# Kernel optimization log

Hardware: AMD Instinct MI355X
Metric: run time of the kernel (lower is better)

## Reference

```python
import jax, jax.numpy as jnp
import numpy as np

B, T, I, H, NC = 128, 512, 128, 512, 100


def setup_inputs() -> dict:
    key = jax.random.key(0)
    ks = jax.random.split(key, 16)
    x = jax.random.randint(ks[0], (B, T, 1), 0, NC + 1)
    # embedding table with padding row 0 zeroed (padding_idx=0)
    emb = (jax.random.normal(ks[1], (NC + 1, I)) * 1.0).at[0].set(0.0)
    # kaiming_normal_ fan_out, sigmoid nonlinearity -> std = 1/sqrt(fan_out)
    sx = 1.0 / np.sqrt(H)
    sc = 1.0 / np.sqrt(H)
    sp = 1.0 / np.sqrt(NC)
    return {
        "x": x,
        "emb": emb,
        "Wfx": jax.random.normal(ks[2], (I, H)) * sx,
        "Wfc": jax.random.normal(ks[3], (H, H)) * sc,
        "bf": jnp.zeros((H,)),
        "Wix": jax.random.normal(ks[4], (I, H)) * sx,
        "Wic": jax.random.normal(ks[5], (H, H)) * sc,
        "bi": jnp.zeros((H,)),
        "Wox": jax.random.normal(ks[6], (I, H)) * sx,
        "Woc": jax.random.normal(ks[7], (H, H)) * sc,
        "bo": jnp.zeros((H,)),
        "Wcx": jax.random.normal(ks[8], (I, H)) * sx,
        "bc": jnp.zeros((H,)),
        "Wph": jax.random.normal(ks[9], (H, NC)) * sp,
        "bp": jnp.zeros((NC,)),
    }


def reference(x, emb, Wfx, Wfc, bf, Wix, Wic, bi, Wox, Woc, bo, Wcx, bc, Wph, bp):
    idx = x[:, :, 0]                      # [B,T] int indices
    xe = emb[idx]                         # [B,T,I] embedded inputs
    h_dim = Wfc.shape[0]
    # Fuse the four input-side GEMMs into one, hoisted out of the recurrence.
    Wx = jnp.concatenate([Wfx, Wix, Wox, Wcx], axis=1)   # [I,4H]
    bx = jnp.concatenate([bf, bi, bo, bc])               # [4H]
    xg = jnp.einsum('bti,ih->bth', xe, Wx) + bx          # [B,T,4H]
    # Fuse the three peephole (cell-state) GEMMs into one per step.
    Wc = jnp.concatenate([Wfc, Wic, Woc], axis=1)        # [H,3H]
    reset = (idx > 0).astype(xg.dtype)                   # [B,T]

    def step(carry, inp):
        C, h = carry
        g, r = inp                        # g: [B,4H], r: [B]
        cg = C @ Wc                       # [B,3H]
        f = jax.nn.sigmoid(g[:, :h_dim] + cg[:, :h_dim])
        i = jax.nn.sigmoid(g[:, h_dim:2 * h_dim] + cg[:, h_dim:2 * h_dim])
        o = jax.nn.sigmoid(g[:, 2 * h_dim:3 * h_dim] + cg[:, 2 * h_dim:])
        c_tilde = jax.nn.sigmoid(g[:, 3 * h_dim:])        # note: sigmoid, not tanh (per source)
        Cn = (c_tilde * i + C * f) * r[:, None]           # reset on padding tokens
        hn = jnp.tanh(Cn) * o
        return (Cn, hn), None

    bsz = xg.shape[0]
    init = (jnp.zeros((bsz, h_dim), xg.dtype), jnp.zeros((bsz, h_dim), xg.dtype))
    xs = (jnp.swapaxes(xg, 0, 1), jnp.swapaxes(reset, 0, 1))  # time-major
    (Cf, hf), _ = jax.lax.scan(step, init, xs)
    p = hf @ Wph + bp                     # [B,num_classes]
    return jax.nn.log_softmax(p, axis=1)
```

## Files before the change

kernel.cpp:

```cpp
#include <hip/hip_runtime.h>
#include <hip/hip_bf16.h>
#include <stdint.h>

#define HD   512
#define ID   128
#define NCLS 100
#define TT   512
#define BB   128
#define NEMB 101
#define THR  512

#define NGRPF 32
#define GWGF  8
#define RPGF  4
#define COLSF 64
#define NGRPB 64
#define GWGB  4
#define RPGB  2
#define COLSB 128

#define CPAD 640
#define CBW  260
#define PROW 2056
#define PSTB 3

#define WS_FLAG 0
#define WS_BAR  4096
#define WS_G    65536
#define WS_C0   (1u * 1024 * 1024)
#define WS_C1   (WS_C0 + 262144)
#define WS_HFB  (WS_C1 + 262144)
#define NBARU   4096
#define NCU     65536

using bf16 = __hip_bfloat16;

__device__ __forceinline__ float b2f(bf16 v) { return __bfloat162float(v); }
__device__ __forceinline__ float sigf(float x) { return 1.0f / (1.0f + expf(-x)); }

__device__ __forceinline__ float cld(const float* p) {
    return __hip_atomic_load(p, __ATOMIC_RELAXED, __HIP_MEMORY_SCOPE_AGENT);
}
__device__ __forceinline__ void cst(float* p, float v) {
    __hip_atomic_store(p, v, __ATOMIC_RELAXED, __HIP_MEMORY_SCOPE_AGENT);
}
__device__ __forceinline__ void cstu(uint32_t* p, uint32_t v) {
    __hip_atomic_store(p, v, __ATOMIC_RELAXED, __HIP_MEMORY_SCOPE_AGENT);
}
__device__ __forceinline__ uint32_t cldu(const uint32_t* p) {
    return __hip_atomic_load(p, __ATOMIC_RELAXED, __HIP_MEMORY_SCOPE_AGENT);
}
__device__ __forceinline__ uint64_t cldu8(const uint64_t* p) {
    return __hip_atomic_load(p, __ATOMIC_RELAXED, __HIP_MEMORY_SCOPE_AGENT);
}

__device__ __forceinline__ uint32_t pkbf(float x, float y) {
    uint32_t u;
    asm("v_cvt_pk_bf16_f32 %0, %1, %2" : "=v"(u) : "v"(x), "v"(y));
    return u;
}
#define DOT2(acc, w, c) \
    asm("v_dot2_f32_bf16 %0, %1, %2, %0" : "+v"(acc) : "v"(w), "v"(c))

template <bool BF>
__device__ __forceinline__ float ldv(const void* p, int i) {
    if constexpr (BF) return b2f(((const bf16*)p)[i]);
    else              return ((const float*)p)[i];
}

__device__ __forceinline__ int cpi(int h) { return (h >> 4) * 20 + (h & 15); }

__device__ __forceinline__ void gbarrier(unsigned* cnt, unsigned* iter, int gwg) {
    __syncthreads();
    if (threadIdx.x == 0) {
        __hip_atomic_fetch_add(cnt, 1u, __ATOMIC_RELAXED, __HIP_MEMORY_SCOPE_AGENT);
        const unsigned tgt = (*iter + 1u) * (unsigned)gwg;
        while (__hip_atomic_load(cnt, __ATOMIC_RELAXED, __HIP_MEMORY_SCOPE_AGENT) < tgt)
            ;
    }
    ++*iter;
    __syncthreads();
}

__global__ void init_k(const uint32_t* __restrict__ emb_raw,
                       int* __restrict__ flag, unsigned* __restrict__ bars,
                       uint32_t* __restrict__ c0, uint32_t* __restrict__ c1) {
    const int t = blockIdx.x * 1024 + threadIdx.x;
    for (int k = t; k < NBARU; k += 8192) bars[k] = 0u;
    for (int k = t; k < NCU; k += 8192) { c0[k] = 0u; c1[k] = 0u; }
    if (t == 0) {
        uint32_t acc = 0;
        for (int i = 64; i < 128; ++i) acc |= emb_raw[i];
        *flag = (acc == 0u) ? 0 : 1;
    }
}

template <bool BF>
__device__ __forceinline__ void build_G_body(
    const void* emb, const void* Wfx, const void* Wix,
    const void* Wox, const void* Wcx,
    const void* bfv, const void* biv, const void* bov, const void* bcv,
    float* G) {
    const int c   = blockIdx.x;
    const int j   = blockIdx.y * 256 + threadIdx.x;
    const int q   = j >> 9;
    const int col = j & 511;
    const void* W  = (q == 0) ? Wfx : (q == 1) ? Wix : (q == 2) ? Wox : Wcx;
    const void* bv = (q == 0) ? bfv : (q == 1) ? biv : (q == 2) ? bov : bcv;
    float acc = ldv<BF>(bv, col);
    #pragma unroll 4
    for (int i = 0; i < ID; ++i)
        acc += ldv<BF>(emb, c * ID + i) * ldv<BF>(W, i * HD + col);
    if (q == 3) acc = sigf(acc);
    G[c * 2048 + j] = acc;
}

__global__ void build_G_k(const int* __restrict__ flag,
                          const void* __restrict__ emb,
                          const void* __restrict__ Wfx, const void* __restrict__ Wix,
                          const void* __restrict__ Wox, const void* __restrict__ Wcx,
                          const void* __restrict__ bfv, const void* __restrict__ biv,
                          const void* __restrict__ bov, const void* __restrict__ bcv,
                          float* __restrict__ G) {
    if (*flag == 0) build_G_body<false>(emb, Wfx, Wix, Wox, Wcx, bfv, biv, bov, bcv, G);
    else            build_G_body<true >(emb, Wfx, Wix, Wox, Wcx, bfv, biv, bov, bcv, G);
}

__global__ __launch_bounds__(THR, 2) void recur_bs(
    const int* __restrict__ flag, const int* __restrict__ x,
    const float* __restrict__ G,
    const void* __restrict__ Wfc, const void* __restrict__ Wic,
    const void* __restrict__ Woc,
    float* __restrict__ C0, float* __restrict__ C1,
    float* __restrict__ Hfb, unsigned* __restrict__ bars)
{
    __shared__ __align__(16) float Cs[RPGF * CPAD];
    __shared__ __align__(16) uint32_t CbS[RPGB * CBW];
    __shared__ __align__(8)  float2 part2[2 * RPGF * PROW];
    __shared__ int idx[RPGF * TT];
    __shared__ int lz[RPGF];

    const int blk = blockIdx.x;
    const int tid = threadIdx.x;
    unsigned bi = 0;
    const int fl = *flag;

    if (fl == 0) {
        const int grp   = blk >> 3;
        const int rank  = blk & 7;
        const int r0    = grp * RPGF;
        const int h0    = rank * COLSF;
        const int cp    = tid & 15;
        const int chunk = tid >> 4;
        unsigned* bar = bars + grp * 32;

        idx[tid]        = x[r0 * TT + tid];
        idx[tid + 512]  = x[r0 * TT + tid + 512];
        idx[tid + 1024] = x[r0 * TT + tid + 1024];
        idx[tid + 1536] = x[r0 * TT + tid + 1536];
        for (int k = tid; k < RPGF * CPAD; k += THR) Cs[k] = 0.0f;
        if (tid < RPGF) lz[tid] = -1;
        __syncthreads();
        #pragma unroll
        for (int r = 0; r < RPGF; ++r)
            if (idx[r * TT + tid] == 0) atomicMax(&lz[r], tid);
        __syncthreads();
        int t0 = TT;
        #pragma unroll
        for (int r = 0; r < RPGF; ++r) t0 = min(t0, lz[r] + 1);

        float wf0[16], wf1[16], wf2[16], wf3[16];
        float wi0[16], wi1[16], wi2[16], wi3[16];
        #pragma unroll
        for (int k = 0; k < 16; ++k) {
            const int hp = chunk * 16 + k;
            wf0[k] = ldv<false>(Wfc, hp * HD + h0 + cp);
            wf1[k] = ldv<false>(Wfc, hp * HD + h0 + cp + 16);
            wf2[k] = ldv<false>(Wfc, hp * HD + h0 + cp + 32);
            wf3[k] = ldv<false>(Wfc, hp * HD + h0 + cp + 48);
            wi0[k] = ldv<false>(Wic, hp * HD + h0 + cp);
            wi1[k] = ldv<false>(Wic, hp * HD + h0 + cp + 16);
            wi2[k] = ldv<false>(Wic, hp * HD + h0 + cp + 32);
            wi3[k] = ldv<false>(Wic, hp * HD + h0 + cp + 48);
        }
        #pragma unroll
        for (int k = 0; k < 16; ++k)
            asm volatile("" : "+v"(wf0[k]), "+v"(wf1[k]), "+v"(wf2[k]), "+v"(wf3[k]),
                              "+v"(wi0[k]), "+v"(wi1[k]), "+v"(wi2[k]), "+v"(wi3[k]));

        const bool isUpd = (tid < COLSF * RPGF);
        const int uc = tid & 63, ur = tid >> 6;
        const int pe = cpi(tid);

        {
            uint32_t* tA = (uint32_t*)((t0 & 1) ? C1 : C0);
            uint32_t* tB = (uint32_t*)((t0 & 1) ? C0 : C1);
            if (isUpd) {
                cstu(tA + (r0 + ur) * HD + h0 + uc, (uint32_t)(t0 & 3));
                cstu(tB + (r0 + ur) * HD + h0 + uc, (uint32_t)((t0 + 3) & 3));
            }
        }
        gbarrier(bar, &bi, GWGF);

        float Creg = 0.0f;
        for (int t = t0; t < TT; ++t) {
            #pragma unroll
            for (int k = 0; k < 16; ++k)
                asm volatile("" : "+v"(wf0[k]), "+v"(wf1[k]), "+v"(wf2[k]), "+v"(wf3[k]),
                                  "+v"(wi0[k]), "+v"(wi1[k]), "+v"(wi2[k]), "+v"(wi3[k]));

            const uint32_t* curT = (const uint32_t*)((t & 1) ? C1 : C0);
            uint32_t*       nxtT = (uint32_t*)((t & 1) ? C0 : C1);

            float gf = 0.f, gi = 0.f, sgc = 0.f;
            int cl = 1;
            if (isUpd) {
                cl = idx[ur * TT + t];
                const float* Gr = G + cl * 2048;
                gf  = Gr[h0 + uc];
                gi  = Gr[512 + h0 + uc];
                sgc = Gr[1536 + h0 + uc];
            }

            {
                const uint32_t* s0 = curT + (r0 + 0) * HD + tid;
                const uint32_t* s1 = curT + (r0 + 1) * HD + tid;
                const uint32_t* s2 = curT + (r0 + 2) * HD + tid;
                const uint32_t* s3 = curT + (r0 + 3) * HD + tid;
                const uint32_t exp = (uint32_t)t & 3u;
                uint32_t w0, w1, w2, w3;
                do { w0 = cldu(s0); } while ((w0 ^ exp) & 3u);
                for (;;) {
                    w1 = cldu(s1); w2 = cldu(s2); w3 = cldu(s3);
                    if ((((w1 ^ exp) | (w2 ^ exp) | (w3 ^ exp)) & 3u) == 0u)
                        break;
                }
                Cs[0 * CPAD + pe] = __uint_as_float(w0 & ~3u);
                Cs[1 * CPAD + pe] = __uint_as_float(w1 & ~3u);
                Cs[2 * CPAD + pe] = __uint_as_float(w2 & ~3u);
                Cs[3 * CPAD + pe] = __uint_as_float(w3 & ~3u);
            }
            asm volatile("s_waitcnt lgkmcnt(0)" ::: "memory");

            float f0[RPGF], f1[RPGF], f2[RPGF], f3[RPGF];
            float i0[RPGF], i1[RPGF], i2[RPGF], i3[RPGF];
            #pragma unroll
            for (int r = 0; r < RPGF; ++r) {
                f0[r] = 0.f; f1[r] = 0.f; f2[r] = 0.f; f3[r] = 0.f;
                i0[r] = 0.f; i1[r] = 0.f; i2[r] = 0.f; i3[r] = 0.f;
            }
            {
                const int cb = chunk * 5;
                #pragma unroll
                for (int j = 0; j < 4; ++j) {
                    #pragma unroll
                    for (int r = 0; r < RPGF; ++r) {
                        const float4 cv = reinterpret_cast<const float4*>(
                            Cs + r * CPAD)[cb + j];
                        f0[r] += wf0[4*j]*cv.x + wf0[4*j+1]*cv.y + wf0[4*j+2]*cv.z + wf0[4*j+3]*cv.w;
                        f1[r] += wf1[4*j]*cv.x + wf1[4*j+1]*cv.y + wf1[4*j+2]*cv.z + wf1[4*j+3]*cv.w;
                        f2[r] += wf2[4*j]*cv.x + wf2[4*j+1]*cv.y + wf2[4*j+2]*cv.z + wf2[4*j+3]*cv.w;
                        f3[r] += wf3[4*j]*cv.x + wf3[4*j+1]*cv.y + wf3[4*j+2]*cv.z + wf3[4*j+3]*cv.w;
                        i0[r] += wi0[4*j]*cv.x + wi0[4*j+1]*cv.y + wi0[4*j+2]*cv.z + wi0[4*j+3]*cv.w;
                        i1[r] += wi1[4*j]*cv.x + wi1[4*j+1]*cv.y + wi1[4*j+2]*cv.z + wi1[4*j+3]*cv.w;
                        i2[r] += wi2[4*j]*cv.x + wi2[4*j+1]*cv.y + wi2[4*j+2]*cv.z + wi2[4*j+3]*cv.w;
                        i3[r] += wi3[4*j]*cv.x + wi3[4*j+1]*cv.y + wi3[4*j+2]*cv.z + wi3[4*j+3]*cv.w;
                    }
                }
            }

            {
                float2* Pb = part2 + (t & 1) * (RPGF * PROW);
                #pragma unroll
                for (int r = 0; r < RPGF; ++r) {
                    float2* Pr = Pb + r * PROW + chunk * 64;
                    Pr[cp]      = make_float2(f0[r], i0[r]);
                    Pr[cp + 16] = make_float2(f1[r], i1[r]);
                    Pr[cp + 32] = make_float2(f2[r], i2[r]);
                    Pr[cp + 48] = make_float2(f3[r], i3[r]);
                }
            }
            __syncthreads();

            if (isUpd) {
                const float2* Pr = part2 + (t & 1) * (RPGF * PROW) + ur * PROW;
                float df = 0.f, di = 0.f;
                #pragma unroll
                for (int ch = 0; ch < 32; ++ch) {
                    const float2 v = Pr[ch * 64 + uc];
                    df += v.x;
                    di += v.y;
                }
                float Cn = sgc * sigf(gi + di) + Creg * sigf(gf + df);
                Cn = (cl > 0) ? Cn : 0.0f;
                Creg = Cn;
                cstu(nxtT + (r0 + ur) * HD + h0 + uc,
                     (__float_as_uint(Cn) & ~3u) | ((uint32_t)(t + 1) & 3u));
            }
        }

        __syncthreads();
        {
            const int oc = tid & 63, och = tid >> 6;
            float ao[RPGF];
            #pragma unroll
            for (int r = 0; r < RPGF; ++r) ao[r] = 0.0f;
            #pragma unroll 4
            for (int k = 0; k < 64; ++k) {
                const int hp = och * 64 + k;
                const int hpp = cpi(hp);
                const float wo = ldv<false>(Woc, hp * HD + h0 + oc);
                #pragma unroll
                for (int r = 0; r < RPGF; ++r)
                    ao[r] += wo * Cs[r * CPAD + hpp];
            }
            {
                #pragma unroll
                for (int r2 = 0; r2 < RPGF / 2; ++r2)
                    part2[r2 * PROW + och * 64 + oc] =
                        make_float2(ao[2 * r2], ao[2 * r2 + 1]);
            }
            __syncthreads();
            if (isUpd) {
                const float2* Pr = part2 + (ur >> 1) * PROW;
                float s = 0.f;
                #pragma unroll
                for (int ch = 0; ch < 8; ++ch) {
                    const float2 v = Pr[ch * 64 + uc];
                    s += (ur & 1) ? v.y : v.x;
                }
                const int cl2 = idx[ur * TT + TT - 1];
                const float o = sigf(G[cl2 * 2048 + 1024 + h0 + uc] + s);
                Hfb[(r0 + ur) * HD + h0 + uc] = tanhf(Creg) * o;
            }
        }
    } else {
        const int grp   = blk >> 2;
        const int rank  = blk & 3;
        const int r0    = grp * RPGB;
        const int h0    = rank * COLSB;
        const int cp    = tid & 31;
        const int chunk = tid >> 5;

        idx[tid]       = x[r0 * TT + tid];
        idx[tid + 512] = x[r0 * TT + tid + 512];
        for (int k = tid; k < RPGB * CBW; k += THR) CbS[k] = 0u;
        if (tid < RPGB) lz[tid] = -1;
        __syncthreads();
        #pragma unroll
        for (int r = 0; r < RPGB; ++r)
            if (idx[r * TT + tid] == 0) atomicMax(&lz[r], tid);
        __syncthreads();
        int t0 = TT;
        #pragma unroll
        for (int r = 0; r < RPGB; ++r) t0 = min(t0, lz[r] + 1);

        const uint16_t* Wfr = (const uint16_t*)Wfc;
        const uint16_t* Wir = (const uint16_t*)Wic;
        uint32_t wf0[16], wf1[16], wf2[16], wf3[16];
        uint32_t wi0[16], wi1[16], wi2[16], wi3[16];
        #pragma unroll
        for (int p = 0; p < 16; ++p) {
            const int hp = chunk * 32 + 2 * p;
            const int b0 = hp * HD + h0 + cp, b1 = (hp + 1) * HD + h0 + cp;
            wf0[p] = (uint32_t)Wfr[b0]      | ((uint32_t)Wfr[b1]      << 16);
            wf1[p] = (uint32_t)Wfr[b0 + 32] | ((uint32_t)Wfr[b1 + 32] << 16);
            wf2[p] = (uint32_t)Wfr[b0 + 64] | ((uint32_t)Wfr[b1 + 64] << 16);
            wf3[p] = (uint32_t)Wfr[b0 + 96] | ((uint32_t)Wfr[b1 + 96] << 16);
            wi0[p] = (uint32_t)Wir[b0]      | ((uint32_t)Wir[b1]      << 16);
            wi1[p] = (uint32_t)Wir[b0 + 32] | ((uint32_t)Wir[b1 + 32] << 16);
            wi2[p] = (uint32_t)Wir[b0 + 64] | ((uint32_t)Wir[b1 + 64] << 16);
            wi3[p] = (uint32_t)Wir[b0 + 96] | ((uint32_t)Wir[b1 + 96] << 16);
        }
        #pragma unroll
        for (int p = 0; p < 16; ++p)
            asm volatile("" : "+v"(wf0[p]), "+v"(wf1[p]), "+v"(wf2[p]), "+v"(wf3[p]),
                              "+v"(wi0[p]), "+v"(wi1[p]), "+v"(wi2[p]), "+v"(wi3[p]));

        const bool isUpd = (tid < COLSB * RPGB);
        const int uc = tid & 127, ur = tid >> 7;

        if (isUpd && t0 > 0) {
            uint32_t* b0 = (uint32_t*)((t0 & 1) ? C1 : C0);
            cstu(b0 + (r0 + ur) * HD + h0 + uc, (uint32_t)t0 & 0xFFFFu);
        }

        float Creg = 0.0f;
        const int srow = tid >> 8;
        const int spr  = tid & 255;

        for (int t = t0; t < TT; ++t) {
            #pragma unroll
            for (int p = 0; p < 16; ++p)
                asm volatile("" : "+v"(wf0[p]), "+v"(wf1[p]), "+v"(wf2[p]), "+v"(wf3[p]),
                                  "+v"(wi0[p]), "+v"(wi1[p]), "+v"(wi2[p]), "+v"(wi3[p]));

            const uint32_t* curT = (const uint32_t*)((t & 1) ? C1 : C0);
            uint32_t*       nxtT = (uint32_t*)((t & 1) ? C0 : C1);

            float gf = 0.f, gi = 0.f, sgc = 0.f;
            int cl = 1;
            if (isUpd) {
                cl = idx[ur * TT + t];
                const float* Gr = G + cl * 2048;
                gf  = Gr[h0 + uc];
                gi  = Gr[512 + h0 + uc];
                sgc = Gr[1536 + h0 + uc];
            }

            {
                const uint64_t* src = (const uint64_t*)(
                    curT + (r0 + srow) * HD + 2 * spr);
                const uint32_t exp = (uint32_t)t & 0xFFFFu;
                uint32_t w0, w1;
                for (;;) {
                    const uint64_t d = cldu8(src);
                    w0 = (uint32_t)d;
                    w1 = (uint32_t)(d >> 32);
                    if ((((w0 ^ exp) | (w1 ^ exp)) & 0xFFFFu) == 0u) break;
                }
                CbS[srow * CBW + spr] = (w0 >> 16) | (w1 & 0xFFFF0000u);
            }
            __syncthreads();

            float f0[RPGB], f1[RPGB], f2[RPGB], f3[RPGB];
            float i0[RPGB], i1[RPGB], i2[RPGB], i3[RPGB];
            #pragma unroll
            for (int r = 0; r < RPGB; ++r) {
                f0[r] = 0.f; f1[r] = 0.f; f2[r] = 0.f; f3[r] = 0.f;
                i0[r] = 0.f; i1[r] = 0.f; i2[r] = 0.f; i3[r] = 0.f;
            }
            {
                const int cb = chunk * 16;
                #pragma unroll
                for (int hh = 0; hh < 4; ++hh) {
                    #pragma unroll
                    for (int r = 0; r < RPGB; ++r) {
                        const uint4 cv = *reinterpret_cast<const uint4*>(
                            CbS + r * CBW + cb + 4 * hh);
                        const int p = 4 * hh;
                        DOT2(f0[r], wf0[p + 0], cv.x); DOT2(f0[r], wf0[p + 1], cv.y);
                        DOT2(f0[r], wf0[p + 2], cv.z); DOT2(f0[r], wf0[p + 3], cv.w);
                        DOT2(f1[r], wf1[p + 0], cv.x); DOT2(f1[r], wf1[p + 1], cv.y);
                        DOT2(f1[r], wf1[p + 2], cv.z); DOT2(f1[r], wf1[p + 3], cv.w);
                        DOT2(f2[r], wf2[p + 0], cv.x); DOT2(f2[r], wf2[p + 1], cv.y);
                        DOT2(f2[r], wf2[p + 2], cv.z); DOT2(f2[r], wf2[p + 3], cv.w);
                        DOT2(f3[r], wf3[p + 0], cv.x); DOT2(f3[r], wf3[p + 1], cv.y);
                        DOT2(f3[r], wf3[p + 2], cv.z); DOT2(f3[r], wf3[p + 3], cv.w);
                        DOT2(i0[r], wi0[p + 0], cv.x); DOT2(i0[r], wi0[p + 1], cv.y);
                        DOT2(i0[r], wi0[p + 2], cv.z); DOT2(i0[r], wi0[p + 3], cv.w);
                        DOT2(i1[r], wi1[p + 0], cv.x); DOT2(i1[r], wi1[p + 1], cv.y);
                        DOT2(i1[r], wi1[p + 2], cv.z); DOT2(i1[r], wi1[p + 3], cv.w);
                        DOT2(i2[r], wi2[p + 0], cv.x); DOT2(i2[r], wi2[p + 1], cv.y);
                        DOT2(i2[r], wi2[p + 2], cv.z); DOT2(i2[r], wi2[p + 3], cv.w);
                        DOT2(i3[r], wi3[p + 0], cv.x); DOT2(i3[r], wi3[p + 1], cv.y);
                        DOT2(i3[r], wi3[p + 2], cv.z); DOT2(i3[r], wi3[p + 3], cv.w);
                    }
                }
            }
            {
                float2* part2b = (float2*)part2;
                float2* p0 = part2b + (chunk * 128 + cp)      * PSTB;
                float2* p1 = part2b + (chunk * 128 + cp + 32) * PSTB;
                float2* p2 = part2b + (chunk * 128 + cp + 64) * PSTB;
                float2* p3 = part2b + (chunk * 128 + cp + 96) * PSTB;
                #pragma unroll
                for (int r = 0; r < RPGB; ++r) {
                    p0[r] = make_float2(f0[r], i0[r]);
                    p1[r] = make_float2(f1[r], i1[r]);
                    p2[r] = make_float2(f2[r], i2[r]);
                    p3[r] = make_float2(f3[r], i3[r]);
                }
            }
            __syncthreads();

            if (isUpd) {
                float df = 0.f, di = 0.f;
                #pragma unroll
                for (int ch = 0; ch < 16; ++ch) {
                    const float2 v = part2[(ch * 128 + uc) * PSTB + ur];
                    df += v.x;
                    di += v.y;
                }
                float Cn = sgc * sigf(gi + di) + Creg * sigf(gf + df);
                Cn = (cl > 0) ? Cn : 0.0f;
                Creg = Cn;
                const uint32_t vb = pkbf(Cn, Cn);
                cstu(nxtT + (r0 + ur) * HD + h0 + uc,
                     (vb << 16) | ((uint32_t)(t + 1) & 0xFFFFu));
            }
        }

        __syncthreads();
        {
            const int rr = tid >> 8, wi = tid & 255;
            const uint32_t w = CbS[rr * CBW + wi];
            Cs[rr * CPAD + cpi(2 * wi)]     = __uint_as_float((w & 0xFFFFu) << 16);
            Cs[rr * CPAD + cpi(2 * wi + 1)] = __uint_as_float(w & 0xFFFF0000u);
            __syncthreads();

            const int oc = tid & 127, och = tid >> 7;
            float ao0 = 0.f, ao1 = 0.f;
            #pragma unroll 4
            for (int k = 0; k < 128; ++k) {
                const int hp  = och * 128 + k;
                const int hpp = cpi(hp);
                const float wo = ldv<true>(Woc, hp * HD + h0 + oc);
                ao0 += wo * Cs[0 * CPAD + hpp];
                ao1 += wo * Cs[1 * CPAD + hpp];
            }
            part2[(och * 128 + oc) * PSTB] = make_float2(ao0, ao1);
            __syncthreads();
            if (isUpd) {
                float s = 0.f;
                #pragma unroll
                for (int ch = 0; ch < 4; ++ch) {
                    const float2 v = part2[(ch * 128 + uc) * PSTB];
                    s += ur ? v.y : v.x;
                }
                const int cl2 = idx[ur * TT + TT - 1];
                const float o = sigf(G[cl2 * 2048 + 1024 + h0 + uc] + s);
                Hfb[(r0 + ur) * HD + h0 + uc] = tanhf(Creg) * o;
            }
        }
    }
}

template <bool BF>
__device__ __forceinline__ void proj_body(
    const float* Hfb, const void* Wph, const void* bp, void* out,
    float* hv, float* p_s, float* lse_s) {
    const int b   = blockIdx.x;
    const int tid = threadIdx.x;

    reinterpret_cast<float4*>(hv)[tid] =
        reinterpret_cast<const float4*>(Hfb + b * HD)[tid];
    __syncthreads();

    if (tid < NCLS) {
        float p = ldv<BF>(bp, tid);
        for (int h = 0; h < HD; ++h)
            p += hv[h] * ldv<BF>(Wph, h * NCLS + tid);
        p_s[tid] = p;
    }
    __syncthreads();
    if (tid == 0) {
        float m = -1e30f;
        for (int n = 0; n < NCLS; ++n) m = fmaxf(m, p_s[n]);
        float sum = 0.0f;
        for (int n = 0; n < NCLS; ++n) sum += expf(p_s[n] - m);
        *lse_s = m + logf(sum);
    }
    __syncthreads();
    if (tid < NCLS) {
        const float v = p_s[tid] - *lse_s;
        if constexpr (BF) ((bf16*)out)[b * NCLS + tid] = __float2bfloat16(v);
        else              ((float*)out)[b * NCLS + tid] = v;
    }
}

__global__ __launch_bounds__(128) void proj_k(
    const int* __restrict__ flag, const float* __restrict__ Hfb,
    const void* __restrict__ Wph, const void* __restrict__ bp,
    void* __restrict__ out)
{
    __shared__ __align__(16) float hv[HD];
    __shared__ float p_s[NCLS];
    __shared__ float lse_s;
    if (*flag == 0) proj_body<false>(Hfb, Wph, bp, out, hv, p_s, &lse_s);
    else            proj_body<true >(Hfb, Wph, bp, out, hv, p_s, &lse_s);
}

extern "C" void kernel_launch(void* const* d_in, const int* in_sizes, int n_in,
                              void* d_out, int out_size, void* d_ws, size_t ws_size,
                              hipStream_t stream) {
    const int*  x   = (const int*)d_in[0];
    const void* emb = d_in[1];
    const void* Wfx = d_in[2];
    const void* Wfc = d_in[3];
    const void* bfv = d_in[4];
    const void* Wix = d_in[5];
    const void* Wic = d_in[6];
    const void* biv = d_in[7];
    const void* Wox = d_in[8];
    const void* Woc = d_in[9];
    const void* bov = d_in[10];
    const void* Wcx = d_in[11];
    const void* bcv = d_in[12];
    const void* Wph = d_in[13];
    const void* bp  = d_in[14];

    int*      flag = (int*)((char*)d_ws + WS_FLAG);
    unsigned* bars = (unsigned*)((char*)d_ws + WS_BAR);
    float*    G    = (float*)((char*)d_ws + WS_G);
    float*    C0   = (float*)((char*)d_ws + WS_C0);
    float*    C1   = (float*)((char*)d_ws + WS_C1);
    float*    Hfb  = (float*)((char*)d_ws + WS_HFB);

    init_k<<<8, 1024, 0, stream>>>((const uint32_t*)emb, flag, bars,
                                   (uint32_t*)C0, (uint32_t*)C1);

    build_G_k<<<dim3(NEMB, 8), 256, 0, stream>>>(flag, emb, Wfx, Wix, Wox, Wcx,
                                                 bfv, biv, bov, bcv, G);

    {
        void* args[] = {(void*)&flag, (void*)&x, (void*)&G,
                        (void*)&Wfc, (void*)&Wic, (void*)&Woc,
                        (void*)&C0, (void*)&C1, (void*)&Hfb, (void*)&bars};
        hipLaunchCooperativeKernel((const void*)recur_bs, dim3(256), dim3(THR),
                                   args, 0, stream);
    }

    proj_k<<<BB, 128, 0, stream>>>(flag, Hfb, Wph, bp, d_out);
}
```

Before: 1.420 ms.

## Fuse init and projection into neighboring kernels to cut launch count

Removes the init kernel by folding the barrier reset and the dtype probe into build_G, and removes the separate projection kernel by running the output projection and log-softmax inside the recurrent cooperative kernel after a final group barrier. The bf16 path now initializes both ping-pong C buffers itself and syncs with a group barrier before starting, instead of relying on the zeroing in init. This cuts launch overhead for two small kernels, but the projection now runs on only one block per group (rank 0), which serializes a little work on fewer CUs.

```diff
diff --git a/kernel.cpp b/kernel.cpp
--- a/kernel.cpp
+++ b/kernel.cpp
@@ -24,14 +24,12 @@
 #define PROW 2056
 #define PSTB 3
 
-#define WS_FLAG 0
 #define WS_BAR  4096
 #define WS_G    65536
 #define WS_C0   (1u * 1024 * 1024)
 #define WS_C1   (WS_C0 + 262144)
 #define WS_HFB  (WS_C1 + 262144)
 #define NBARU   4096
-#define NCU     65536
 
 using bf16 = __hip_bfloat16;
 
@@ -82,17 +80,14 @@
     __syncthreads();
 }
 
-__global__ void init_k(const uint32_t* __restrict__ emb_raw,
-                       int* __restrict__ flag, unsigned* __restrict__ bars,
-                       uint32_t* __restrict__ c0, uint32_t* __restrict__ c1) {
-    const int t = blockIdx.x * 1024 + threadIdx.x;
-    for (int k = t; k < NBARU; k += 8192) bars[k] = 0u;
-    for (int k = t; k < NCU; k += 8192) { c0[k] = 0u; c1[k] = 0u; }
-    if (t == 0) {
-        uint32_t acc = 0;
-        for (int i = 64; i < 128; ++i) acc |= emb_raw[i];
-        *flag = (acc == 0u) ? 0 : 1;
-    }
+__device__ __forceinline__ int probe_flag(const uint32_t* emb_raw,
+                                          uint32_t* accS) {
+    if (threadIdx.x == 0) *accS = 0u;
+    __syncthreads();
+    if (threadIdx.x < 64 && emb_raw[64 + threadIdx.x] != 0u)
+        atomicOr(accS, 1u);
+    __syncthreads();
+    return (*accS != 0u) ? 1 : 0;
 }
 
 template <bool BF>
@@ -115,35 +110,42 @@
     G[c * 2048 + j] = acc;
 }
 
-__global__ void build_G_k(const int* __restrict__ flag,
-                          const void* __restrict__ emb,
+__global__ void build_G_k(const void* __restrict__ emb,
                           const void* __restrict__ Wfx, const void* __restrict__ Wix,
                           const void* __restrict__ Wox, const void* __restrict__ Wcx,
                           const void* __restrict__ bfv, const void* __restrict__ biv,
                           const void* __restrict__ bov, const void* __restrict__ bcv,
-                          float* __restrict__ G) {
-    if (*flag == 0) build_G_body<false>(emb, Wfx, Wix, Wox, Wcx, bfv, biv, bov, bcv, G);
-    else            build_G_body<true >(emb, Wfx, Wix, Wox, Wcx, bfv, biv, bov, bcv, G);
-}
-
-__global__ __launch_bounds__(THR, 2) void recur_bs(
-    const int* __restrict__ flag, const int* __restrict__ x,
-    const float* __restrict__ G,
+                          float* __restrict__ G, unsigned* __restrict__ bars) {
+    __shared__ uint32_t accS;
+    if (blockIdx.x == 0 && blockIdx.y == 0)
+        for (int k = threadIdx.x; k < NBARU; k += 256) bars[k] = 0u;
+    const int fl = probe_flag((const uint32_t*)emb, &accS);
+    if (fl == 0) build_G_body<false>(emb, Wfx, Wix, Wox, Wcx, bfv, biv, bov, bcv, G);
+    else         build_G_body<true >(emb, Wfx, Wix, Wox, Wcx, bfv, biv, bov, bcv, G);
+}
+
+__global__ __launch_bounds__(THR, 2) void recur_fused(
+    const int* __restrict__ x, const float* __restrict__ G,
     const void* __restrict__ Wfc, const void* __restrict__ Wic,
     const void* __restrict__ Woc,
     float* __restrict__ C0, float* __restrict__ C1,
-    float* __restrict__ Hfb, unsigned* __restrict__ bars)
+    float* __restrict__ Hfb, unsigned* __restrict__ bars,
+    const void* __restrict__ emb,
+    const void* __restrict__ Wph, const void* __restrict__ bp,
+    void* __restrict__ out)
 {
     __shared__ __align__(16) float Cs[RPGF * CPAD];
     __shared__ __align__(16) uint32_t CbS[RPGB * CBW];
     __shared__ __align__(8)  float2 part2[2 * RPGF * PROW];
     __shared__ int idx[RPGF * TT];
     __shared__ int lz[RPGF];
+    __shared__ uint32_t accS;
+    __shared__ float lseS[RPGF];
 
     const int blk = blockIdx.x;
     const int tid = threadIdx.x;
     unsigned bi = 0;
-    const int fl = *flag;
+    const int fl = probe_flag((const uint32_t*)emb, &accS);
 
     if (fl == 0) {
         const int grp   = blk >> 3;
@@ -331,8 +333,40 @@
                 }
                 const int cl2 = idx[ur * TT + TT - 1];
                 const float o = sigf(G[cl2 * 2048 + 1024 + h0 + uc] + s);
-                Hfb[(r0 + ur) * HD + h0 + uc] = tanhf(Creg) * o;
-            }
+                cst(&Hfb[(r0 + ur) * HD + h0 + uc], tanhf(Creg) * o);
+            }
+        }
+
+        gbarrier(bar, &bi, GWGF);
+        if (rank == 0) {
+            float* hv = (float*)part2;
+            hv[0 * 512 + tid] = cld(Hfb + (r0 + 0) * HD + tid);
+            hv[1 * 512 + tid] = cld(Hfb + (r0 + 1) * HD + tid);
+            hv[2 * 512 + tid] = cld(Hfb + (r0 + 2) * HD + tid);
+            hv[3 * 512 + tid] = cld(Hfb + (r0 + 3) * HD + tid);
+            __syncthreads();
+            const int row = tid >> 7, c = tid & 127;
+            float p = -1e30f;
+            if (c < NCLS) {
+                p = ldv<false>(bp, c);
+                const float* hr = hv + row * 512;
+                for (int h = 0; h < HD; ++h)
+                    p += hr[h] * ldv<false>(Wph, h * NCLS + c);
+            }
+            float* ps = hv + 4 * 512;
+            ps[row * 128 + c] = p;
+            __syncthreads();
+            if (c == 0) {
+                const float* pr = ps + row * 128;
+                float m = -1e30f;
+                for (int n = 0; n < NCLS; ++n) m = fmaxf(m, pr[n]);
+                float sum = 0.0f;
+                for (int n = 0; n < NCLS; ++n) sum += expf(pr[n] - m);
+                lseS[row] = m + logf(sum);
+            }
+            __syncthreads();
+            if (c < NCLS)
+                ((float*)out)[(r0 + row) * NCLS + c] = ps[row * 128 + c] - lseS[row];
         }
     } else {
         const int grp   = blk >> 2;
@@ -341,6 +375,7 @@
         const int h0    = rank * COLSB;
         const int cp    = tid & 31;
         const int chunk = tid >> 5;
+        unsigned* bar = bars + grp * 32;
 
         idx[tid]       = x[r0 * TT + tid];
         idx[tid + 512] = x[r0 * TT + tid + 512];
@@ -380,10 +415,13 @@
         const bool isUpd = (tid < COLSB * RPGB);
         const int uc = tid & 127, ur = tid >> 7;
 
-        if (isUpd && t0 > 0) {
-            uint32_t* b0 = (uint32_t*)((t0 & 1) ? C1 : C0);
-            cstu(b0 + (r0 + ur) * HD + h0 + uc, (uint32_t)t0 & 0xFFFFu);
-        }
+        if (isUpd) {
+            uint32_t* bufA = (uint32_t*)((t0 & 1) ? C1 : C0);
+            uint32_t* bufB = (uint32_t*)((t0 & 1) ? C0 : C1);
+            cstu(bufA + (r0 + ur) * HD + h0 + uc, (uint32_t)t0 & 0xFFFFu);
+            cstu(bufB + (r0 + ur) * HD + h0 + uc, 0xFFFFu);
+        }
+        gbarrier(bar, &bi, GWGB);
 
         float Creg = 0.0f;
         const int srow = tid >> 8;
@@ -520,55 +558,41 @@
                 }
                 const int cl2 = idx[ur * TT + TT - 1];
                 const float o = sigf(G[cl2 * 2048 + 1024 + h0 + uc] + s);
-                Hfb[(r0 + ur) * HD + h0 + uc] = tanhf(Creg) * o;
-            }
+                cst(&Hfb[(r0 + ur) * HD + h0 + uc], tanhf(Creg) * o);
+            }
+        }
+
+        gbarrier(bar, &bi, GWGB);
+        if (rank == 0) {
+            float* hv = (float*)part2;
+            hv[0 * 512 + tid] = cld(Hfb + (r0 + 0) * HD + tid);
+            hv[1 * 512 + tid] = cld(Hfb + (r0 + 1) * HD + tid);
+            __syncthreads();
+            const int row = tid >> 8, c = tid & 255;
+            float p = -1e30f;
+            if (c < NCLS) {
+                p = ldv<true>(bp, c);
+                const float* hr = hv + row * 512;
+                for (int h = 0; h < HD; ++h)
+                    p += hr[h] * ldv<true>(Wph, h * NCLS + c);
+            }
+            float* ps = hv + 2 * 512;
+            ps[row * 256 + c] = p;
+            __syncthreads();
+            if (c == 0) {
+                const float* pr = ps + row * 256;
+                float m = -1e30f;
+                for (int n = 0; n < NCLS; ++n) m = fmaxf(m, pr[n]);
+                float sum = 0.0f;
+                for (int n = 0; n < NCLS; ++n) sum += expf(pr[n] - m);
+                lseS[row] = m + logf(sum);
+            }
+            __syncthreads();
+            if (c < NCLS)
+                ((bf16*)out)[(r0 + row) * NCLS + c] =
+                    __float2bfloat16(ps[row * 256 + c] - lseS[row]);
         }
     }
-}
-
-template <bool BF>
-__device__ __forceinline__ void proj_body(
-    const float* Hfb, const void* Wph, const void* bp, void* out,
-    float* hv, float* p_s, float* lse_s) {
-    const int b   = blockIdx.x;
-    const int tid = threadIdx.x;
-
-    reinterpret_cast<float4*>(hv)[tid] =
-        reinterpret_cast<const float4*>(Hfb + b * HD)[tid];
-    __syncthreads();
-
-    if (tid < NCLS) {
-        float p = ldv<BF>(bp, tid);
-        for (int h = 0; h < HD; ++h)
-            p += hv[h] * ldv<BF>(Wph, h * NCLS + tid);
-        p_s[tid] = p;
-    }
-    __syncthreads();
-    if (tid == 0) {
-        float m = -1e30f;
-        for (int n = 0; n < NCLS; ++n) m = fmaxf(m, p_s[n]);
-        float sum = 0.0f;
-        for (int n = 0; n < NCLS; ++n) sum += expf(p_s[n] - m);
-        *lse_s = m + logf(sum);
-    }
-    __syncthreads();
-    if (tid < NCLS) {
-        const float v = p_s[tid] - *lse_s;
-        if constexpr (BF) ((bf16*)out)[b * NCLS + tid] = __float2bfloat16(v);
-        else              ((float*)out)[b * NCLS + tid] = v;
-    }
-}
-
-__global__ __launch_bounds__(128) void proj_k(
-    const int* __restrict__ flag, const float* __restrict__ Hfb,
-    const void* __restrict__ Wph, const void* __restrict__ bp,
-    void* __restrict__ out)
-{
-    __shared__ __align__(16) float hv[HD];
-    __shared__ float p_s[NCLS];
-    __shared__ float lse_s;
-    if (*flag == 0) proj_body<false>(Hfb, Wph, bp, out, hv, p_s, &lse_s);
-    else            proj_body<true >(Hfb, Wph, bp, out, hv, p_s, &lse_s);
 }
 
 extern "C" void kernel_launch(void* const* d_in, const int* in_sizes, int n_in,
@@ -590,26 +614,21 @@
     const void* Wph = d_in[13];
     const void* bp  = d_in[14];
 
-    int*      flag = (int*)((char*)d_ws + WS_FLAG);
     unsigned* bars = (unsigned*)((char*)d_ws + WS_BAR);
     float*    G    = (float*)((char*)d_ws + WS_G);
     float*    C0   = (float*)((char*)d_ws + WS_C0);
     float*    C1   = (float*)((char*)d_ws + WS_C1);
     float*    Hfb  = (float*)((char*)d_ws + WS_HFB);
 
-    init_k<<<8, 1024, 0, stream>>>((const uint32_t*)emb, flag, bars,
-                                   (uint32_t*)C0, (uint32_t*)C1);
-
-    build_G_k<<<dim3(NEMB, 8), 256, 0, stream>>>(flag, emb, Wfx, Wix, Wox, Wcx,
-                                                 bfv, biv, bov, bcv, G);
+    build_G_k<<<dim3(NEMB, 8), 256, 0, stream>>>(emb, Wfx, Wix, Wox, Wcx,
+                                                 bfv, biv, bov, bcv, G, bars);
 
     {
-        void* args[] = {(void*)&flag, (void*)&x, (void*)&G,
+        void* args[] = {(void*)&x, (void*)&G,
                         (void*)&Wfc, (void*)&Wic, (void*)&Woc,
-                        (void*)&C0, (void*)&C1, (void*)&Hfb, (void*)&bars};
-        hipLaunchCooperativeKernel((const void*)recur_bs, dim3(256), dim3(THR),
+                        (void*)&C0, (void*)&C1, (void*)&Hfb, (void*)&bars,
+                        (void*)&emb, (void*)&Wph, (void*)&bp, (void*)&d_out};
+        hipLaunchCooperativeKernel((const void*)recur_fused, dim3(256), dim3(THR),
                                    args, 0, stream);
     }
-
-    proj_k<<<BB, 128, 0, stream>>>(flag, Hfb, Wph, bp, d_out);
-}
+}
```

After: 1.540 ms. 1.08x slower.
